# Performance work log

Hardware: AMD Instinct MI355X
Metric: run time of the kernel (lower is better)

## Reference

```python
import jax, jax.numpy as jnp
import numpy as np
import math

B = 4096
INPUT_SIZE = 2048
HIDDEN_SIZE = 2048


def setup_inputs() -> dict:
    key = jax.random.key(0)
    ks = jax.random.split(key, 7)
    std = 1.0 / math.sqrt(HIDDEN_SIZE)
    u = lambda k, shape: jax.random.uniform(k, shape, jnp.float32, -std, std)
    return {
        "input": jax.random.normal(ks[0], (B, INPUT_SIZE), jnp.float32),
        "hx": jax.random.normal(ks[1], (B, HIDDEN_SIZE), jnp.float32),
        "cx": jax.random.normal(ks[2], (B, HIDDEN_SIZE), jnp.float32),
        "W_x2h": u(ks[3], (4 * HIDDEN_SIZE, INPUT_SIZE)),
        "b_x2h": u(ks[4], (4 * HIDDEN_SIZE,)),
        "W_h2h": u(ks[5], (4 * HIDDEN_SIZE, HIDDEN_SIZE)),
        "b_h2h": u(ks[6], (4 * HIDDEN_SIZE,)),
    }


def reference(input, hx, cx, W_x2h, b_x2h, W_h2h, b_h2h):
    # gates: [B, 4H] = x @ W_x2h^T + b + h @ W_h2h^T + b
    gates = input @ W_x2h.T + b_x2h + hx @ W_h2h.T + b_h2h
    H = HIDDEN_SIZE
    ft = jax.nn.sigmoid(gates[:, 0 * H:1 * H])
    it = jax.nn.sigmoid(gates[:, 1 * H:2 * H])
    ct = jnp.tanh(gates[:, 2 * H:3 * H])
    ot = jax.nn.sigmoid(gates[:, 3 * H:4 * H])
    cy = ft * cx + it * ct
    hy = ot * jnp.tanh(cy)
    return (hy, cy)
```

## Files before the change

kernel.cpp:

```cpp
#include <hip/hip_runtime.h>
#include <hip/hip_bf16.h>


#define BATCH 4096
#define HID   2048
#define KDIM  2048
#define K4    4096
#define LDK   72

typedef __attribute__((ext_vector_type(8))) short  short8;
typedef __attribute__((ext_vector_type(4))) float  f32x4;

__device__ __forceinline__ float sigm(float x)  { return 1.f / (1.f + __expf(-x)); }
__device__ __forceinline__ float tanhx(float x) { return 2.f / (1.f + __expf(-2.f * x)) - 1.f; }

__device__ __forceinline__ uint2 pk_bf16x4(float4 v) {
  __hip_bfloat162 lo = __float22bfloat162_rn(make_float2(v.x, v.y));
  __hip_bfloat162 hi = __float22bfloat162_rn(make_float2(v.z, v.w));
  uint2 r;
  r.x = *(unsigned*)&lo;
  r.y = *(unsigned*)&hi;
  return r;
}

__device__ __forceinline__ void gload16(const void* g, void* l) {
  __builtin_amdgcn_global_load_lds(
      (const __attribute__((address_space(1))) unsigned int*)g,
      (__attribute__((address_space(3))) unsigned int*)l, 16, 0, 0);
}

#define BAR()  asm volatile("s_barrier" ::: "memory")
#define VMC(n) asm volatile("s_waitcnt vmcnt(" #n ")" ::: "memory")

__global__ __launch_bounds__(256) void conv_a(const float* __restrict__ X,
                                              const float* __restrict__ Hx,
                                              short* __restrict__ A) {
  const int gid = blockIdx.x * 256 + threadIdx.x;
  const int m   = gid >> 9;
  const int pos = (gid & 511) << 3;
  const float* src = (pos < KDIM) ? X  + (size_t)m * KDIM + pos
                                  : Hx + (size_t)m * KDIM + (pos - KDIM);
  float4 v0 = *(const float4*)src;
  float4 v1 = *(const float4*)(src + 4);
  uint2 p0 = pk_bf16x4(v0), p1 = pk_bf16x4(v1);
  uint4 o; o.x = p0.x; o.y = p0.y; o.z = p1.x; o.w = p1.y;
  *(uint4*)(A + (size_t)gid * 8) = o;
}

__global__ __launch_bounds__(256) void conv_b(const float* __restrict__ Wx,
                                              const float* __restrict__ Wh,
                                              short* __restrict__ Bm) {
  const int gid = blockIdx.x * 256 + threadIdx.x;
  const int jp  = gid >> 9;
  const int pos = (gid & 511) << 3;
  const int srow = (jp & 3) * HID + (jp >> 2);
  const float* src = (pos < KDIM) ? Wx + (size_t)srow * KDIM + pos
                                  : Wh + (size_t)srow * KDIM + (pos - KDIM);
  float4 v0 = *(const float4*)src;
  float4 v1 = *(const float4*)(src + 4);
  uint2 p0 = pk_bf16x4(v0), p1 = pk_bf16x4(v1);
  uint4 o; o.x = p0.x; o.y = p0.y; o.z = p1.x; o.w = p1.y;
  *(uint4*)(Bm + (size_t)gid * 8) = o;
}

__device__ __forceinline__ void lda4(short8 (&dst)[8], const short* base,
                                     int arow, int sx0, int sx1, int mfb) {
  #pragma unroll
  for (int u = 0; u < 4; ++u) {
    dst[u]     = *(const short8*)&base[arow + (mfb + u) * 1024 + sx0];
    dst[4 + u] = *(const short8*)&base[arow + (mfb + u) * 1024 + sx1];
  }
}
__device__ __forceinline__ void ldb2(short8 (&dst)[4], const short* base,
                                     int brow, int sx0, int sx1, int nfb) {
  #pragma unroll
  for (int v = 0; v < 2; ++v) {
    dst[v]     = *(const short8*)&base[brow + (nfb + v) * 1024 + sx0];
    dst[2 + v] = *(const short8*)&base[brow + (nfb + v) * 1024 + sx1];
  }
}
__device__ __forceinline__ void mmq(f32x4 (&acc)[8][4], const short8 (&A)[8],
                                    const short8 (&B)[4], int MB, int NB) {
  __builtin_amdgcn_s_setprio(1);
  #pragma unroll
  for (int ks = 0; ks < 2; ++ks)
    #pragma unroll
    for (int u = 0; u < 4; ++u)
      #pragma unroll
      for (int v = 0; v < 2; ++v)
        acc[MB + u][NB + v] = __builtin_amdgcn_mfma_f32_16x16x32_bf16(
            A[ks * 4 + u], B[ks * 2 + v], acc[MB + u][NB + v], 0, 0, 0);
  __builtin_amdgcn_s_setprio(0);
}

__global__ __launch_bounds__(512, 2) void lstm_mm8(
    const short* __restrict__ A, const short* __restrict__ Bm,
    const float* __restrict__ Cx,
    const float* __restrict__ bx, const float* __restrict__ bh,
    float* __restrict__ Hy, float* __restrict__ Cy)
{
  __shared__ __align__(16) short A_sh[2 * 16384];
  __shared__ __align__(16) short B_sh[2 * 16384];

  const int tid  = threadIdx.x;
  const int wv   = tid >> 6;
  const int lane = tid & 63;
  const int quad = lane >> 4;
  const int ln   = lane & 15;
  const int wm   = wv >> 2;
  const int wn   = wv & 3;
  const int m0   = blockIdx.x * 256;
  const int j0   = blockIdx.y * 256;
  const int h0   = blockIdx.y * 64;

  f32x4 acc[8][4];
  #pragma unroll
  for (int a = 0; a < 8; ++a)
    #pragma unroll
    for (int b = 0; b < 4; ++b)
      acc[a][b] = (f32x4){0.f, 0.f, 0.f, 0.f};

  const int l8  = lane >> 3;
  const int swz = ((lane & 7) ^ (l8 & 7)) << 3;
  const short* aG = A  + (size_t)(m0 + l8) * K4 + swz;
  const short* bG = Bm + (size_t)(j0 + l8) * K4 + swz;

  #define STAGE_A(d, h, tau) do {                                             \
    gload16(aG + ((size_t)((h)*128 + wv*16    )) * K4 + (tau)*64,             \
            &A_sh[(d)*16384 + (h)*8192 + wv*1024]);                           \
    gload16(aG + ((size_t)((h)*128 + wv*16 + 8)) * K4 + (tau)*64,             \
            &A_sh[(d)*16384 + (h)*8192 + wv*1024 + 512]);                     \
  } while (0)
  #define STAGE_B(d, h, tau) do {                                             \
    gload16(bG + ((size_t)((h)*128 + wv*16    )) * K4 + (tau)*64,             \
            &B_sh[(d)*16384 + (h)*8192 + wv*1024]);                           \
    gload16(bG + ((size_t)((h)*128 + wv*16 + 8)) * K4 + (tau)*64,             \
            &B_sh[(d)*16384 + (h)*8192 + wv*1024 + 512]);                     \
  } while (0)
  #define STAGE_TILE(d, tau) do {                                             \
    STAGE_A(d, 0, tau); STAGE_A(d, 1, tau);                                   \
    STAGE_B(d, 0, tau); STAGE_B(d, 1, tau);                                   \
  } while (0)

  const int arow = (wm * 128 + ln) * 64;
  const int brow = (wn * 64  + ln) * 64;
  const int sx0  = ((0 + quad) ^ (ln & 7)) << 3;
  const int sx1  = ((4 + quad) ^ (ln & 7)) << 3;

  STAGE_TILE(0, 0);
  STAGE_TILE(1, 1);
  VMC(8);
  BAR();

  short8 aQ0[8], aQ1[8], bLo[4], bHi[4];

  #define HALF(D, stageIt, d, tauNext, gateN) do {                            \
    lda4(aQ0, &A_sh[D], arow, sx0, sx1, 0);                                   \
    ldb2(bLo, &B_sh[D], brow, sx0, sx1, 0);                                   \
    lda4(aQ1, &A_sh[D], arow, sx0, sx1, 4);                                   \
    ldb2(bHi, &B_sh[D], brow, sx0, sx1, 2);                                   \
    mmq(acc, aQ0, bLo, 0, 0);                                                 \
    mmq(acc, aQ1, bLo, 4, 0);                                                 \
    mmq(acc, aQ1, bHi, 4, 2);                                                 \
    mmq(acc, aQ0, bHi, 0, 2);                                                 \
    BAR();                                                                    \
    if (stageIt) { STAGE_TILE(d, tauNext); VMC(8); } else { VMC(gateN); }     \
    BAR();                                                                    \
  } while (0)

  #pragma unroll 1
  for (int i = 0; i < 32; ++i) {
    const bool nl = (i != 31);
    HALF(0,     nl, 0, 2 * i + 2, 0);
    HALF(16384, nl, 1, 2 * i + 3, 0);
  }
  #undef HALF
  #undef STAGE_TILE
  #undef STAGE_B
  #undef STAGE_A

  const int g = lane & 3;
  float biasv[4];
  int   hgs[4];
  #pragma unroll
  for (int nf = 0; nf < 4; ++nf) {
    int c  = wn * 64 + nf * 16 + ln;
    int hg = h0 + (c >> 2);
    hgs[nf] = hg;
    int j = g * HID + hg;
    biasv[nf] = bx[j] + bh[j];
  }
  #pragma unroll
  for (int mf = 0; mf < 8; ++mf) {
    #pragma unroll
    for (int r = 0; r < 4; ++r) {
      int mrow = m0 + wm * 128 + mf * 16 + quad * 4 + r;
      #pragma unroll
      for (int nf = 0; nf < 4; ++nf) {
        float v   = acc[mf][nf][r] + biasv[nf];
        float act = (g == 2) ? tanhx(v) : sigm(v);
        float y1 = __shfl_xor(act, 1);
        float y2 = __shfl_xor(act, 2);
        float y3 = __shfl_xor(act, 3);
        float ft = (g == 0) ? act : ((g == 1) ? y1 : ((g == 2) ? y2 : y3));
        float it = (g == 1) ? act : ((g == 0) ? y1 : ((g == 3) ? y2 : y3));
        float gt = (g == 2) ? act : ((g == 3) ? y1 : ((g == 0) ? y2 : y3));
        float ot = (g == 3) ? act : ((g == 2) ? y1 : ((g == 1) ? y2 : y3));
        if (g < 2) {
          size_t off = (size_t)mrow * HID + hgs[nf];
          float cxv = Cx[off];
          float cyv = ft * cxv + it * gt;
          if (g == 0) Hy[off] = ot * tanhx(cyv);
          else        Cy[off] = cyv;
        }
      }
    }
  }
}

__global__ __launch_bounds__(256) void lstm_cell_fallback(
    const float* __restrict__ X, const float* __restrict__ Hx,
    const float* __restrict__ Cx,
    const float* __restrict__ Wx, const float* __restrict__ bx,
    const float* __restrict__ Wh, const float* __restrict__ bh,
    float* __restrict__ Hy, float* __restrict__ Cy)
{
  __shared__ __align__(16) short A_lds[128 * LDK];
  __shared__ __align__(16) short B_lds[128 * LDK];

  const int tid  = threadIdx.x;
  const int wv   = tid >> 6;
  const int lane = tid & 63;
  const int quad = lane >> 4;
  const int ln   = lane & 15;
  const int wm   = wv >> 1;
  const int wn   = wv & 1;
  const int m0   = blockIdx.x * 128;
  const int h0   = blockIdx.y * 32;

  f32x4 acc[4][4];
  #pragma unroll
  for (int a = 0; a < 4; ++a)
    #pragma unroll
    for (int b = 0; b < 4; ++b)
      acc[a][b] = (f32x4){0.f, 0.f, 0.f, 0.f};

  const int rA  = tid >> 4;
  const int kc4 = (tid & 15) * 4;
  size_t aoff[8], boff[8];
  int    lrow[8];
  #pragma unroll
  for (int q = 0; q < 8; ++q) {
    int row  = q * 16 + rA;
    lrow[q]  = row;
    aoff[q]  = (size_t)(m0 + row) * KDIM + kc4;
    int wrow = (row & 3) * HID + h0 + (row >> 2);
    boff[q]  = (size_t)wrow * KDIM + kc4;
  }

  const int NT = 2 * (KDIM / 64);
  float4 areg[8], breg[8];
  #pragma unroll
  for (int q = 0; q < 8; ++q) {
    areg[q] = *(const float4*)(X  + aoff[q]);
    breg[q] = *(const float4*)(Wx + boff[q]);
  }

  for (int t = 0; t < NT; ++t) {
    __syncthreads();
    #pragma unroll
    for (int q = 0; q < 8; ++q) {
      *(uint2*)&A_lds[lrow[q] * LDK + kc4] = pk_bf16x4(areg[q]);
      *(uint2*)&B_lds[lrow[q] * LDK + kc4] = pk_bf16x4(breg[q]);
    }
    __syncthreads();
    if (t + 1 < NT) {
      const float* Ap = (t + 1 < 32) ? X  : Hx;
      const float* Wp = (t + 1 < 32) ? Wx : Wh;
      const int k0 = ((t + 1) & 31) * 64;
      #pragma unroll
      for (int q = 0; q < 8; ++q) {
        areg[q] = *(const float4*)(Ap + aoff[q] + k0);
        breg[q] = *(const float4*)(Wp + boff[q] + k0);
      }
    }
    #pragma unroll
    for (int ks = 0; ks < 2; ++ks) {
      short8 af[4], bfv[4];
      #pragma unroll
      for (int u = 0; u < 4; ++u)
        af[u] = *(const short8*)&A_lds[(wm * 64 + u * 16 + ln) * LDK + ks * 32 + quad * 8];
      #pragma unroll
      for (int u = 0; u < 4; ++u)
        bfv[u] = *(const short8*)&B_lds[(wn * 64 + u * 16 + ln) * LDK + ks * 32 + quad * 8];
      #pragma unroll
      for (int tm = 0; tm < 4; ++tm)
        #pragma unroll
        for (int tn = 0; tn < 4; ++tn)
          acc[tm][tn] = __builtin_amdgcn_mfma_f32_16x16x32_bf16(
              af[tm], bfv[tn], acc[tm][tn], 0, 0, 0);
    }
  }

  const int g = lane & 3;
  float biasv[4];
  int   hgs[4];
  #pragma unroll
  for (int tn = 0; tn < 4; ++tn) {
    int c  = wn * 64 + tn * 16 + ln;
    int hg = h0 + (c >> 2);
    hgs[tn] = hg;
    int j = g * HID + hg;
    biasv[tn] = bx[j] + bh[j];
  }
  #pragma unroll
  for (int tm = 0; tm < 4; ++tm) {
    #pragma unroll
    for (int r = 0; r < 4; ++r) {
      int mrow = m0 + wm * 64 + tm * 16 + quad * 4 + r;
      #pragma unroll
      for (int tn = 0; tn < 4; ++tn) {
        float v   = acc[tm][tn][r] + biasv[tn];
        float act = (g == 2) ? tanhx(v) : sigm(v);
        float y1 = __shfl_xor(act, 1);
        float y2 = __shfl_xor(act, 2);
        float y3 = __shfl_xor(act, 3);
        float ft = (g == 0) ? act : ((g == 1) ? y1 : ((g == 2) ? y2 : y3));
        float it = (g == 1) ? act : ((g == 0) ? y1 : ((g == 3) ? y2 : y3));
        float gt = (g == 2) ? act : ((g == 3) ? y1 : ((g == 0) ? y2 : y3));
        float ot = (g == 3) ? act : ((g == 2) ? y1 : ((g == 1) ? y2 : y3));
        if (g < 2) {
          size_t off = (size_t)mrow * HID + hgs[tn];
          float cxv = Cx[off];
          float cyv = ft * cxv + it * gt;
          if (g == 0) Hy[off] = ot * tanhx(cyv);
          else        Cy[off] = cyv;
        }
      }
    }
  }
}

extern "C" void kernel_launch(void* const* d_in, const int* in_sizes, int n_in,
                              void* d_out, int out_size, void* d_ws, size_t ws_size,
                              hipStream_t stream) {
  const float* X  = (const float*)d_in[0];
  const float* Hx = (const float*)d_in[1];
  const float* Cx = (const float*)d_in[2];
  const float* Wx = (const float*)d_in[3];
  const float* bx = (const float*)d_in[4];
  const float* Wh = (const float*)d_in[5];
  const float* bh = (const float*)d_in[6];
  float*       Hy = (float*)d_out;
  float*       Cy = Hy + (size_t)BATCH * HID;

  const size_t needA = (size_t)BATCH * K4 * sizeof(short);
  const size_t needB = (size_t)(4 * HID) * K4 * sizeof(short);

  if (d_ws != nullptr && ws_size >= needA + needB) {
    short* Abf = (short*)d_ws;
    short* Bbf = (short*)((char*)d_ws + needA);
    conv_a<<<dim3((BATCH * (K4 / 8)) / 256), dim3(256), 0, stream>>>(X, Hx, Abf);
    conv_b<<<dim3((4 * HID * (K4 / 8)) / 256), dim3(256), 0, stream>>>(Wx, Wh, Bbf);
    dim3 grid(BATCH / 256, (4 * HID) / 256, 1);
    lstm_mm8<<<grid, dim3(512, 1, 1), 0, stream>>>(Abf, Bbf, Cx, bx, bh, Hy, Cy);
  } else {
    dim3 grid(BATCH / 128, HID / 32, 1);
    lstm_cell_fallback<<<grid, dim3(256, 1, 1), 0, stream>>>(X, Hx, Cx, Wx, bx, Wh, bh, Hy, Cy);
  }
}
```

Measured before the change: 576.7 us.

## Pre-tile and pre-swizzle bf16 operands into contiguous LDS-ready blocks; fuse conversion kernels

The two fp32-to-bf16 conversion kernels become one pack kernel. It writes A and B in a tiled layout where each 256-row by 64-k stage, with the XOR swizzle applied, is a single contiguous 32 KB chunk. The GEMM's global-to-LDS loads then read fully contiguous memory, replacing 16-byte pieces strided across many rows, and one kernel launch is removed. In exchange the pack kernel's fp32 reads become scattered, which may lower conversion bandwidth.

```diff
diff --git a/kernel.cpp b/kernel.cpp
--- a/kernel.cpp
+++ b/kernel.cpp
@@ -32,35 +32,42 @@
 #define BAR()  asm volatile("s_barrier" ::: "memory")
 #define VMC(n) asm volatile("s_waitcnt vmcnt(" #n ")" ::: "memory")
 
-__global__ __launch_bounds__(256) void conv_a(const float* __restrict__ X,
-                                              const float* __restrict__ Hx,
-                                              short* __restrict__ A) {
+#define ACHUNKS (16 * 64 * 2048)
+#define BCHUNKS (32 * 64 * 2048)
+
+__global__ __launch_bounds__(256) void conv_pack(
+    const float* __restrict__ X,  const float* __restrict__ Hx,
+    const float* __restrict__ Wx, const float* __restrict__ Wh,
+    short* __restrict__ At, short* __restrict__ Bt) {
   const int gid = blockIdx.x * 256 + threadIdx.x;
-  const int m   = gid >> 9;
-  const int pos = (gid & 511) << 3;
-  const float* src = (pos < KDIM) ? X  + (size_t)m * KDIM + pos
-                                  : Hx + (size_t)m * KDIM + (pos - KDIM);
+  const bool isA = gid < ACHUNKS;
+  const int c  = isA ? gid : gid - ACHUNKS;
+  const int t  = c >> 11;
+  const int w  = c & 2047;
+  const int bt = t >> 6;
+  const int kt = t & 63;
+  const int h  = w >> 10;
+  const int wvv= (w >> 7) & 7;
+  const int q  = (w >> 6) & 1;
+  const int l8 = (w >> 3) & 7;
+  const int p  = w & 7;
+  const int row = bt * 256 + h * 128 + wvv * 16 + q * 8 + l8;
+  const int k   = kt * 64 + ((p ^ l8) << 3);
+  const float* src;
+  if (isA) {
+    src = (k < KDIM) ? X + (size_t)row * KDIM + k
+                     : Hx + (size_t)row * KDIM + (k - KDIM);
+  } else {
+    const int srow = (row & 3) * HID + (row >> 2);
+    src = (k < KDIM) ? Wx + (size_t)srow * KDIM + k
+                     : Wh + (size_t)srow * KDIM + (k - KDIM);
+  }
   float4 v0 = *(const float4*)src;
   float4 v1 = *(const float4*)(src + 4);
   uint2 p0 = pk_bf16x4(v0), p1 = pk_bf16x4(v1);
   uint4 o; o.x = p0.x; o.y = p0.y; o.z = p1.x; o.w = p1.y;
-  *(uint4*)(A + (size_t)gid * 8) = o;
-}
-
-__global__ __launch_bounds__(256) void conv_b(const float* __restrict__ Wx,
-                                              const float* __restrict__ Wh,
-                                              short* __restrict__ Bm) {
-  const int gid = blockIdx.x * 256 + threadIdx.x;
-  const int jp  = gid >> 9;
-  const int pos = (gid & 511) << 3;
-  const int srow = (jp & 3) * HID + (jp >> 2);
-  const float* src = (pos < KDIM) ? Wx + (size_t)srow * KDIM + pos
-                                  : Wh + (size_t)srow * KDIM + (pos - KDIM);
-  float4 v0 = *(const float4*)src;
-  float4 v1 = *(const float4*)(src + 4);
-  uint2 p0 = pk_bf16x4(v0), p1 = pk_bf16x4(v1);
-  uint4 o; o.x = p0.x; o.y = p0.y; o.z = p1.x; o.w = p1.y;
-  *(uint4*)(Bm + (size_t)gid * 8) = o;
+  short* dst = isA ? At : Bt;
+  *(uint4*)(dst + (size_t)c * 8) = o;
 }
 
 __device__ __forceinline__ void lda4(short8 (&dst)[8], const short* base,
@@ -94,7 +101,7 @@
 }
 
 __global__ __launch_bounds__(512, 2) void lstm_mm8(
-    const short* __restrict__ A, const short* __restrict__ Bm,
+    const short* __restrict__ At, const short* __restrict__ Bt,
     const float* __restrict__ Cx,
     const float* __restrict__ bx, const float* __restrict__ bh,
     float* __restrict__ Hy, float* __restrict__ Cy)
@@ -110,7 +117,6 @@
   const int wm   = wv >> 2;
   const int wn   = wv & 3;
   const int m0   = blockIdx.x * 256;
-  const int j0   = blockIdx.y * 256;
   const int h0   = blockIdx.y * 64;
 
   f32x4 acc[8][4];
@@ -120,21 +126,19 @@
     for (int b = 0; b < 4; ++b)
       acc[a][b] = (f32x4){0.f, 0.f, 0.f, 0.f};
 
-  const int l8  = lane >> 3;
-  const int swz = ((lane & 7) ^ (l8 & 7)) << 3;
-  const short* aG = A  + (size_t)(m0 + l8) * K4 + swz;
-  const short* bG = Bm + (size_t)(j0 + l8) * K4 + swz;
+  const short* aT = At + ((size_t)blockIdx.x * 64) * 16384 + lane * 8;
+  const short* bT = Bt + ((size_t)blockIdx.y * 64) * 16384 + lane * 8;
 
   #define STAGE_A(d, h, tau) do {                                             \
-    gload16(aG + ((size_t)((h)*128 + wv*16    )) * K4 + (tau)*64,             \
+    gload16(aT + (size_t)(tau) * 16384 + (h) * 8192 + wv * 1024,              \
             &A_sh[(d)*16384 + (h)*8192 + wv*1024]);                           \
-    gload16(aG + ((size_t)((h)*128 + wv*16 + 8)) * K4 + (tau)*64,             \
+    gload16(aT + (size_t)(tau) * 16384 + (h) * 8192 + wv * 1024 + 512,        \
             &A_sh[(d)*16384 + (h)*8192 + wv*1024 + 512]);                     \
   } while (0)
   #define STAGE_B(d, h, tau) do {                                             \
-    gload16(bG + ((size_t)((h)*128 + wv*16    )) * K4 + (tau)*64,             \
+    gload16(bT + (size_t)(tau) * 16384 + (h) * 8192 + wv * 1024,              \
             &B_sh[(d)*16384 + (h)*8192 + wv*1024]);                           \
-    gload16(bG + ((size_t)((h)*128 + wv*16 + 8)) * K4 + (tau)*64,             \
+    gload16(bT + (size_t)(tau) * 16384 + (h) * 8192 + wv * 1024 + 512,        \
             &B_sh[(d)*16384 + (h)*8192 + wv*1024 + 512]);                     \
   } while (0)
   #define STAGE_TILE(d, tau) do {                                             \
@@ -354,14 +358,14 @@
   float*       Hy = (float*)d_out;
   float*       Cy = Hy + (size_t)BATCH * HID;
 
-  const size_t needA = (size_t)BATCH * K4 * sizeof(short);
-  const size_t needB = (size_t)(4 * HID) * K4 * sizeof(short);
+  const size_t needA = (size_t)ACHUNKS * 8 * sizeof(short);
+  const size_t needB = (size_t)BCHUNKS * 8 * sizeof(short);
 
   if (d_ws != nullptr && ws_size >= needA + needB) {
     short* Abf = (short*)d_ws;
     short* Bbf = (short*)((char*)d_ws + needA);
-    conv_a<<<dim3((BATCH * (K4 / 8)) / 256), dim3(256), 0, stream>>>(X, Hx, Abf);
-    conv_b<<<dim3((4 * HID * (K4 / 8)) / 256), dim3(256), 0, stream>>>(Wx, Wh, Bbf);
+    conv_pack<<<dim3((ACHUNKS + BCHUNKS) / 256), dim3(256), 0, stream>>>(
+        X, Hx, Wx, Wh, Abf, Bbf);
     dim3 grid(BATCH / 256, (4 * HID) / 256, 1);
     lstm_mm8<<<grid, dim3(512, 1, 1), 0, stream>>>(Abf, Bbf, Cx, bx, bh, Hy, Cy);
   } else {
```

New measurement: 576.2 us. About the same (-0.1%).
